# Optimization experiments

Hardware: AMD Instinct MI355X
Metric: run time of the kernel (lower is better)

Reference implementation:

```python
import jax, jax.numpy as jnp
import numpy as np

N_EMBD = 1024
N_HEAD = 16

def _lin_params(key, fan_in, fan_out):
    kw, kb = jax.random.split(key)
    bound = 1.0 / np.sqrt(fan_in)
    W = jax.random.uniform(kw, (fan_in, fan_out), minval=-bound, maxval=bound, dtype=jnp.float32)
    b = jax.random.uniform(kb, (fan_out,), minval=-bound, maxval=bound, dtype=jnp.float32)
    return W, b

def setup_inputs() -> dict:
    key = jax.random.key(0)
    ks = jax.random.split(key, 6)
    x = jax.random.normal(ks[0], (2, 2048, N_EMBD), dtype=jnp.float32)
    W_attn, b_attn = _lin_params(ks[1], N_EMBD, 3 * N_EMBD)
    W_proj, b_proj = _lin_params(ks[2], N_EMBD, N_EMBD)
    W_fc, b_fc = _lin_params(ks[3], N_EMBD, 4 * N_EMBD)
    W_fc2, b_fc2 = _lin_params(ks[4], 4 * N_EMBD, N_EMBD)
    ln1_g = jnp.ones((N_EMBD,), jnp.float32); ln1_b = jnp.zeros((N_EMBD,), jnp.float32)
    ln2_g = jnp.ones((N_EMBD,), jnp.float32); ln2_b = jnp.zeros((N_EMBD,), jnp.float32)
    return {"x": x, "W_attn": W_attn, "b_attn": b_attn, "W_proj": W_proj, "b_proj": b_proj,
            "W_fc": W_fc, "b_fc": b_fc, "W_fc2": W_fc2, "b_fc2": b_fc2,
            "ln1_g": ln1_g, "ln1_b": ln1_b, "ln2_g": ln2_g, "ln2_b": ln2_b}

def _layernorm(x, g, b, eps=1e-5):
    mu = jnp.mean(x, axis=-1, keepdims=True)
    var = jnp.var(x, axis=-1, keepdims=True)
    return (x - mu) * jax.lax.rsqrt(var + eps) * g + b

def _attention(x, W_attn, b_attn, W_proj, b_proj):
    B, T, C = x.shape
    hd = C // N_HEAD
    qkv = x @ W_attn + b_attn                      # [B,T,3C]
    q, k, v = jnp.split(qkv, 3, axis=-1)
    # [B,T,C] -> [B,H,T,hd]
    q = q.reshape(B, T, N_HEAD, hd).transpose(0, 2, 1, 3)
    k = k.reshape(B, T, N_HEAD, hd).transpose(0, 2, 1, 3)
    v = v.reshape(B, T, N_HEAD, hd).transpose(0, 2, 1, 3)
    att = jnp.einsum('bhqd,bhkd->bhqk', q, k) * (1.0 / np.sqrt(hd))
    causal = jnp.tril(jnp.ones((T, T), bool))
    att = jnp.where(causal[None, None], att, -jnp.inf)
    att = jax.nn.softmax(att, axis=-1)
    y = jnp.einsum('bhqk,bhkd->bhqd', att, v)      # [B,H,T,hd]
    y = y.transpose(0, 2, 1, 3).reshape(B, T, C)
    return y @ W_proj + b_proj

def _mlp(x, W_fc, b_fc, W_fc2, b_fc2):
    h = jax.nn.gelu(x @ W_fc + b_fc, approximate=False)
    return h @ W_fc2 + b_fc2

def reference(x, W_attn, b_attn, W_proj, b_proj, W_fc, b_fc, W_fc2, b_fc2,
              ln1_g, ln1_b, ln2_g, ln2_b):
    x = x + _attention(_layernorm(x, ln1_g, ln1_b), W_attn, b_attn, W_proj, b_proj)
    x = x + _mlp(_layernorm(x, ln2_g, ln2_b), W_fc, b_fc, W_fc2, b_fc2)
    return x
```

## Files before the change

kernel.cpp:

```cpp
#include <hip/hip_runtime.h>
#include <cstdint>
#include <cstddef>


typedef unsigned short u16;
typedef short bf16x8 __attribute__((ext_vector_type(8)));
typedef float f32x4 __attribute__((ext_vector_type(4)));

#define C_EMBD 1024
#define T_SEQ  2048
#define N_BATCH 2
#define N_HEADS 16
#define HEAD_D 64
#define M_TOK  4096
#define Q_SCALE 0.18033688011112042f

__device__ __forceinline__ u16 f2b(float f) {
  union { float f; unsigned u; } v; v.f = f;
  unsigned r = (v.u + 0x7fffu + ((v.u >> 16) & 1u)) >> 16;
  return (u16)r;
}
__device__ __forceinline__ float b2f(u16 u) {
  union { unsigned u; float f; } v; v.u = ((unsigned)u) << 16;
  return v.f;
}
__device__ __forceinline__ unsigned pk2(float a, float b) {
  union { float f; unsigned u; } x, y; x.f = a; y.f = b;
  return __builtin_amdgcn_perm(y.u, x.u, 0x07060302u);
}
__device__ __forceinline__ void load_lds16(const void* g, void* l) {
  __builtin_amdgcn_global_load_lds(
      (const __attribute__((address_space(1))) void*)g,
      (__attribute__((address_space(3))) void*)l, 16, 0, 0);
}
__device__ __forceinline__ float gelu_fast(float x) {
  const float p = x * __builtin_fmaf(0.044715f * x, x, 1.0f);
  const float t = __builtin_amdgcn_exp2f(2.3021859215f * p);
  return x * t * __builtin_amdgcn_rcpf(t + 1.0f);
}

__global__ __launch_bounds__(256) void transpose_cast(
    const float* __restrict__ W, u16* __restrict__ Wt, int K, int N) {
  __shared__ float tile[32][33];
  const int n0 = blockIdx.x * 32, k0 = blockIdx.y * 32;
  const int tx = threadIdx.x & 31, ty = threadIdx.x >> 5;
#pragma unroll
  for (int i = 0; i < 32; i += 8)
    tile[ty + i][tx] = W[(size_t)(k0 + ty + i) * N + n0 + tx];
  __syncthreads();
#pragma unroll
  for (int i = 0; i < 32; i += 8)
    Wt[(size_t)(n0 + ty + i) * K + k0 + tx] = f2b(tile[tx][ty + i]);
}

__global__ __launch_bounds__(256) void ln_cast(
    const float* __restrict__ X, const float* __restrict__ g,
    const float* __restrict__ b, u16* __restrict__ Y) {
  const int row = blockIdx.x;
  const int tid = threadIdx.x;
  const float4 v = ((const float4*)(X + (size_t)row * C_EMBD))[tid];
  float s = v.x + v.y + v.z + v.w;
  float ss = v.x * v.x + v.y * v.y + v.z * v.z + v.w * v.w;
#pragma unroll
  for (int off = 32; off > 0; off >>= 1) {
    s += __shfl_down(s, off, 64);
    ss += __shfl_down(ss, off, 64);
  }
  __shared__ float red[8];
  __shared__ float stats[2];
  const int wave = tid >> 6, lane = tid & 63;
  if (lane == 0) { red[wave] = s; red[4 + wave] = ss; }
  __syncthreads();
  if (tid == 0) {
    float S = red[0] + red[1] + red[2] + red[3];
    float SS = red[4] + red[5] + red[6] + red[7];
    float mu = S * (1.0f / C_EMBD);
    float var = SS * (1.0f / C_EMBD) - mu * mu;
    stats[0] = mu;
    stats[1] = rsqrtf(var + 1e-5f);
  }
  __syncthreads();
  const float mu = stats[0], rs = stats[1];
  const float4 gv = ((const float4*)g)[tid];
  const float4 bv = ((const float4*)b)[tid];
  ushort4 o;
  o.x = f2b((v.x - mu) * rs * gv.x + bv.x);
  o.y = f2b((v.y - mu) * rs * gv.y + bv.y);
  o.z = f2b((v.z - mu) * rs * gv.z + bv.z);
  o.w = f2b((v.w - mu) * rs * gv.w + bv.w);
  ((ushort4*)(Y + (size_t)row * C_EMBD))[tid] = o;
}

enum { EPI_BF16 = 0, EPI_GELU_BF16 = 2, EPI_PART = 3, EPI_QKV = 4 };

template <int EPI, int SPLIT>
__global__ __launch_bounds__(256) void gemm_bt(
    const u16* __restrict__ A, const u16* __restrict__ Bt,
    const float* __restrict__ bias,
    void* __restrict__ Cout, void* __restrict__ Cout2, void* __restrict__ Cout3,
    int M, int N, int K) {
  __shared__ u16 As[128 * 64];
  __shared__ u16 Bs[128 * 64];
  const int tid = threadIdx.x;
  const int wave = tid >> 6, lane = tid & 63;
  const int quad = lane >> 4, l16 = lane & 15;
  const int sw = l16 & 7;
  const int m0 = blockIdx.y * 128, n0 = blockIdx.x * 128;
  const int wm = (wave >> 1) * 64, wn = (wave & 1) * 64;

  f32x4 acc[4][4] = {};

  const int kTiles = (K >> 6) / SPLIT;
  const int kt0 = (SPLIT == 2) ? (int)blockIdx.z * kTiles : 0;
  for (int kt = kt0; kt < kt0 + kTiles; ++kt) {
    const int k0 = kt << 6;
#pragma unroll
    for (int i = 0; i < 4; ++i) {
      const int c = tid + i * 256;
      const int row = c >> 3, gc = ((c & 7) ^ (row & 7)) * 8;
      load_lds16(A + (size_t)(m0 + row) * K + k0 + gc, &As[c * 8]);
    }
#pragma unroll
    for (int i = 0; i < 4; ++i) {
      const int c = tid + i * 256;
      const int row = c >> 3, gc = ((c & 7) ^ (row & 7)) * 8;
      load_lds16(Bt + (size_t)(n0 + row) * K + k0 + gc, &Bs[c * 8]);
    }
    __syncthreads();
#pragma unroll
    for (int ks = 0; ks < 2; ++ks) {
      bf16x8 aF[4], bF[4];
#pragma unroll
      for (int t = 0; t < 4; ++t) {
        aF[t] = *(const bf16x8*)
            &As[(wm + t * 16 + l16) * 64 + (((ks * 4 + quad) ^ sw) * 8)];
        bF[t] = *(const bf16x8*)
            &Bs[(wn + t * 16 + l16) * 64 + (((ks * 4 + quad) ^ sw) * 8)];
      }
#pragma unroll
      for (int tm = 0; tm < 4; ++tm)
#pragma unroll
        for (int tn = 0; tn < 4; ++tn)
          acc[tm][tn] = __builtin_amdgcn_mfma_f32_16x16x32_bf16(
              bF[tn], aF[tm], acc[tm][tn], 0, 0, 0);
    }
    __syncthreads();
  }

  float* Pz = (float*)((SPLIT == 2 && blockIdx.z == 1) ? Cout2 : Cout);
#pragma unroll
  for (int tm = 0; tm < 4; ++tm) {
    const int row = m0 + wm + tm * 16 + l16;
#pragma unroll
    for (int tn = 0; tn < 4; ++tn) {
      const int col = n0 + wn + tn * 16 + quad * 4;
      if constexpr (EPI == EPI_PART) {
        *(float4*)&Pz[(size_t)row * N + col] = *(float4*)&acc[tm][tn];
      } else if constexpr (EPI == EPI_QKV) {
        const int bb = row >> 11, t = row & (T_SEQ - 1);
        const float4 bz = *(const float4*)&bias[col];
        float v0 = acc[tm][tn][0] + bz.x, v1 = acc[tm][tn][1] + bz.y;
        float v2 = acc[tm][tn][2] + bz.z, v3 = acc[tm][tn][3] + bz.w;
        const int sec = col >> 10;
        const int h = (col & 1023) >> 6, d4 = col & 63;
        const int bh = bb * N_HEADS + h;
        if (sec == 0) {
          ushort4 o;
          o.x = f2b(v0 * Q_SCALE); o.y = f2b(v1 * Q_SCALE);
          o.z = f2b(v2 * Q_SCALE); o.w = f2b(v3 * Q_SCALE);
          *(ushort4*)&((u16*)Cout)[((size_t)bh * T_SEQ + t) * HEAD_D + d4] = o;
        } else if (sec == 1) {
          ushort4 o;
          o.x = f2b(v0); o.y = f2b(v1); o.z = f2b(v2); o.w = f2b(v3);
          *(ushort4*)&((u16*)Cout2)[((size_t)bh * T_SEQ + t) * HEAD_D + d4] = o;
        } else {
          u16* vp = (u16*)Cout3 + ((size_t)bh * HEAD_D + d4) * T_SEQ + t;
          vp[0] = f2b(v0); vp[T_SEQ] = f2b(v1);
          vp[2 * T_SEQ] = f2b(v2); vp[3 * T_SEQ] = f2b(v3);
        }
      } else {
        const float4 bz = *(const float4*)&bias[col];
        float v0 = acc[tm][tn][0] + bz.x, v1 = acc[tm][tn][1] + bz.y;
        float v2 = acc[tm][tn][2] + bz.z, v3 = acc[tm][tn][3] + bz.w;
        if constexpr (EPI == EPI_GELU_BF16) {
          v0 = gelu_fast(v0); v1 = gelu_fast(v1);
          v2 = gelu_fast(v2); v3 = gelu_fast(v3);
        }
        ushort4 o;
        o.x = f2b(v0); o.y = f2b(v1); o.z = f2b(v2); o.w = f2b(v3);
        *(ushort4*)&((u16*)Cout)[(size_t)row * N + col] = o;
      }
    }
  }
}

__global__ __launch_bounds__(256) void reduce_add(
    const float* __restrict__ P0, const float* __restrict__ P1,
    const float* __restrict__ bias, const float* __restrict__ res,
    float* __restrict__ out) {
  const int idx = blockIdx.x * 256 + threadIdx.x;
  const float4 a = ((const float4*)P0)[idx];
  const float4 b = ((const float4*)P1)[idx];
  const float4 c = ((const float4*)res)[idx];
  const float4 g = ((const float4*)bias)[idx & 255];
  float4 o;
  o.x = a.x + b.x + c.x + g.x;
  o.y = a.y + b.y + c.y + g.y;
  o.z = a.z + b.z + c.z + g.z;
  o.w = a.w + b.w + c.w + g.w;
  ((float4*)out)[idx] = o;
}

__global__ __launch_bounds__(256) void attn_fwd(
    const u16* __restrict__ Q, const u16* __restrict__ Kb,
    const u16* __restrict__ Vt, u16* __restrict__ Y) {
  const int bh = blockIdx.y;
  const int pair = blockIdx.x;
  const int nqt = (int)(T_SEQ / 64);
  const int tid = threadIdx.x;
  const int wave = tid >> 6, lane = tid & 63;
  const int quad = lane >> 4, l16 = lane & 15;
  const int sw = l16 & 7;
  const u16* Qp = Q + (size_t)bh * T_SEQ * HEAD_D;
  const u16* Kp = Kb + (size_t)bh * T_SEQ * HEAD_D;
  const u16* Vp = Vt + (size_t)bh * HEAD_D * T_SEQ;

  __shared__ u16 Ks[2][64 * 64];
  __shared__ u16 Vs[2][64 * 64];
  __shared__ u16 Pl[4][16 * 72];

  const int c1 = tid, c2 = tid + 256;
  const int r1 = c1 >> 3, g1 = ((c1 & 7) ^ (r1 & 7)) * 8;
  const int r2 = c2 >> 3, g2 = ((c2 & 7) ^ (r2 & 7)) * 8;
  const size_t kO1 = (size_t)r1 * HEAD_D + g1, kO2 = (size_t)r2 * HEAD_D + g2;
  const size_t vO1 = (size_t)r1 * T_SEQ + g1, vO2 = (size_t)r2 * T_SEQ + g2;
  u16* const dK1[2] = {&Ks[0][c1 * 8], &Ks[1][c1 * 8]};
  u16* const dK2[2] = {&Ks[0][c2 * 8], &Ks[1][c2 * 8]};
  u16* const dV1[2] = {&Vs[0][c1 * 8], &Vs[1][c1 * 8]};
  u16* const dV2[2] = {&Vs[0][c2 * 8], &Vs[1][c2 * 8]};

  auto stageK = [&](int bb, int k0) {
    const u16* base = Kp + (size_t)k0 * HEAD_D;
    load_lds16(base + kO1, dK1[bb]);
    load_lds16(base + kO2, dK2[bb]);
  };
  auto stageV = [&](int bb, int k0) {
    const u16* base = Vp + k0;
    load_lds16(base + vO1, dV1[bb]);
    load_lds16(base + vO2, dV2[bb]);
  };

  const int b = bh >> 4, h = bh & 15;

#pragma unroll 1
  for (int phase = 0; phase < 2; ++phase) {
    const int qb = phase == 0 ? (nqt - 1 - pair) : pair;
    const int q0 = qb * 64;
    const int qglob = q0 + wave * 16 + l16;

    if (phase == 1) __syncthreads();

    bf16x8 qF[2];
    qF[0] = *(const bf16x8*)&Qp[(size_t)qglob * HEAD_D + quad * 8];
    qF[1] = *(const bf16x8*)&Qp[(size_t)qglob * HEAD_D + 32 + quad * 8];

    f32x4 o[4] = {};
    float mrun = -3e38f, lrun = 0.0f;

    stageK(0, 0);
    stageV(0, 0);

    int buf = 0;
    for (int kb = 0; kb <= qb; ++kb) {
      const int k0 = kb * 64;
      __syncthreads();
      if (kb < qb) {
        stageK(buf ^ 1, k0 + 64);
        stageV(buf ^ 1, k0 + 64);
      }
      f32x4 st[4] = {};
#pragma unroll
      for (int ks = 0; ks < 2; ++ks) {
#pragma unroll
        for (int nt = 0; nt < 4; ++nt) {
          bf16x8 kF = *(const bf16x8*)
              &Ks[buf][(nt * 16 + l16) * 64 + (((ks * 4 + quad) ^ sw) * 8)];
          st[nt] = __builtin_amdgcn_mfma_f32_16x16x32_bf16(kF, qF[ks], st[nt],
                                                           0, 0, 0);
        }
      }
      if (kb == qb) {
#pragma unroll
        for (int nt = 0; nt < 4; ++nt) {
#pragma unroll
          for (int r = 0; r < 4; ++r) {
            const int key = k0 + nt * 16 + quad * 4 + r;
            if (key > qglob) st[nt][r] = -3e38f;
          }
        }
      }
      float m = st[0][0];
#pragma unroll
      for (int nt = 0; nt < 4; ++nt)
#pragma unroll
        for (int r = 0; r < 4; ++r) m = fmaxf(m, st[nt][r]);
      m = fmaxf(m, __shfl_xor(m, 16, 64));
      m = fmaxf(m, __shfl_xor(m, 32, 64));
      const float nm = fmaxf(mrun, m);
      const float alpha = __builtin_amdgcn_exp2f(mrun - nm);
      mrun = nm;
      float sum = 0.0f;
#pragma unroll
      for (int nt = 0; nt < 4; ++nt)
#pragma unroll
        for (int r = 0; r < 4; ++r) {
          const float p = __builtin_amdgcn_exp2f(st[nt][r] - nm);
          st[nt][r] = p;
          sum += p;
        }
      sum += __shfl_xor(sum, 16, 64);
      sum += __shfl_xor(sum, 32, 64);
      lrun = lrun * alpha + sum;
#pragma unroll
      for (int nt = 0; nt < 4; ++nt)
#pragma unroll
        for (int r = 0; r < 4; ++r) o[nt][r] *= alpha;
#pragma unroll
      for (int nt = 0; nt < 4; ++nt) {
        uint2 pk;
        pk.x = pk2(st[nt][0], st[nt][1]);
        pk.y = pk2(st[nt][2], st[nt][3]);
        *(uint2*)&Pl[wave][l16 * 72 + nt * 16 + quad * 4] = pk;
      }
#pragma unroll
      for (int ks = 0; ks < 2; ++ks) {
        bf16x8 aP = *(const bf16x8*)&Pl[wave][l16 * 72 + ks * 32 + quad * 8];
#pragma unroll
        for (int nt = 0; nt < 4; ++nt) {
          bf16x8 vF = *(const bf16x8*)
              &Vs[buf][(nt * 16 + l16) * 64 + (((ks * 4 + quad) ^ sw) * 8)];
          o[nt] =
              __builtin_amdgcn_mfma_f32_16x16x32_bf16(vF, aP, o[nt], 0, 0, 0);
        }
      }
      buf ^= 1;
    }

    const float rl = 1.0f / lrun;
    u16* yp = Y + ((size_t)(b * T_SEQ + qglob)) * C_EMBD + h * HEAD_D;
#pragma unroll
    for (int nt = 0; nt < 4; ++nt) {
      ushort4 ov;
      ov.x = f2b(o[nt][0] * rl); ov.y = f2b(o[nt][1] * rl);
      ov.z = f2b(o[nt][2] * rl); ov.w = f2b(o[nt][3] * rl);
      *(ushort4*)&yp[nt * 16 + quad * 4] = ov;
    }
  }
}

extern "C" void kernel_launch(void* const* d_in, const int* in_sizes, int n_in,
                              void* d_out, int out_size, void* d_ws,
                              size_t ws_size, hipStream_t stream) {
  const float* x      = (const float*)d_in[0];
  const float* W_attn = (const float*)d_in[1];
  const float* b_attn = (const float*)d_in[2];
  const float* W_proj = (const float*)d_in[3];
  const float* b_proj = (const float*)d_in[4];
  const float* W_fc   = (const float*)d_in[5];
  const float* b_fc   = (const float*)d_in[6];
  const float* W_fc2  = (const float*)d_in[7];
  const float* b_fc2  = (const float*)d_in[8];
  const float* ln1_g  = (const float*)d_in[9];
  const float* ln1_b  = (const float*)d_in[10];
  const float* ln2_g  = (const float*)d_in[11];
  const float* ln2_b  = (const float*)d_in[12];

  u16* wqkvT = (u16*)d_ws;
  u16* wprojT = wqkvT + (size_t)3072 * 1024;
  u16* wfcT  = wprojT + (size_t)1024 * 1024;
  u16* wfc2T = wfcT + (size_t)4096 * 1024;
  u16* Abuf  = wfc2T + (size_t)1024 * 4096;
  float* x1  = (float*)(Abuf + (size_t)M_TOK * C_EMBD);
  u16* hbuf  = (u16*)(x1 + (size_t)M_TOK * C_EMBD);
  float* projP = (float*)hbuf;
  u16* Qb    = hbuf + (size_t)M_TOK * 4096;
  u16* Kbuf  = Qb + (size_t)32 * T_SEQ * HEAD_D;
  u16* Vtb   = Kbuf + (size_t)32 * T_SEQ * HEAD_D;
  float* fc2P1 = (float*)Qb;

  const dim3 blk(256);

  transpose_cast<<<dim3(3072 / 32, 1024 / 32), blk, 0, stream>>>(W_attn, wqkvT, 1024, 3072);
  transpose_cast<<<dim3(1024 / 32, 1024 / 32), blk, 0, stream>>>(W_proj, wprojT, 1024, 1024);
  transpose_cast<<<dim3(4096 / 32, 1024 / 32), blk, 0, stream>>>(W_fc, wfcT, 1024, 4096);
  transpose_cast<<<dim3(1024 / 32, 4096 / 32), blk, 0, stream>>>(W_fc2, wfc2T, 4096, 1024);

  ln_cast<<<M_TOK, blk, 0, stream>>>(x, ln1_g, ln1_b, Abuf);

  gemm_bt<EPI_QKV, 1><<<dim3(3072 / 128, M_TOK / 128), blk, 0, stream>>>(
      Abuf, wqkvT, b_attn, Qb, Kbuf, Vtb, M_TOK, 3072, 1024);

  attn_fwd<<<dim3(T_SEQ / 128, 32), blk, 0, stream>>>(Qb, Kbuf, Vtb, Abuf);

  gemm_bt<EPI_PART, 2><<<dim3(1024 / 128, M_TOK / 128, 2), blk, 0, stream>>>(
      Abuf, wprojT, nullptr, projP, projP + (size_t)M_TOK * C_EMBD, nullptr,
      M_TOK, 1024, 1024);
  reduce_add<<<M_TOK * C_EMBD / 1024, blk, 0, stream>>>(
      projP, projP + (size_t)M_TOK * C_EMBD, b_proj, x, x1);

  ln_cast<<<M_TOK, blk, 0, stream>>>(x1, ln2_g, ln2_b, Abuf);

  gemm_bt<EPI_GELU_BF16, 1><<<dim3(4096 / 128, M_TOK / 128), blk, 0, stream>>>(
      Abuf, wfcT, b_fc, hbuf, nullptr, nullptr, M_TOK, 4096, 1024);

  gemm_bt<EPI_PART, 2><<<dim3(1024 / 128, M_TOK / 128, 2), blk, 0, stream>>>(
      hbuf, wfc2T, nullptr, d_out, fc2P1, nullptr, M_TOK, 1024, 4096);
  reduce_add<<<M_TOK * C_EMBD / 1024, blk, 0, stream>>>(
      (const float*)d_out, fc2P1, b_fc2, x1, (float*)d_out);
}
```

Measured before the change: 362.2 us.

## Fuse split-K reduce with LayerNorm and group GEMM tiles along M

```diff
diff --git a/kernel.cpp b/kernel.cpp
--- a/kernel.cpp
+++ b/kernel.cpp
@@ -91,6 +91,56 @@
   ((ushort4*)(Y + (size_t)row * C_EMBD))[tid] = o;
 }
 
+__global__ __launch_bounds__(256) void ln_reduce_cast(
+    const float* __restrict__ P0, const float* __restrict__ P1,
+    const float* __restrict__ bias, const float* __restrict__ res,
+    const float* __restrict__ g, const float* __restrict__ b,
+    float* __restrict__ X1, u16* __restrict__ Y) {
+  const int row = blockIdx.x;
+  const int tid = threadIdx.x;
+  const size_t base = (size_t)row * C_EMBD;
+  const float4 p0 = ((const float4*)(P0 + base))[tid];
+  const float4 p1 = ((const float4*)(P1 + base))[tid];
+  const float4 rr = ((const float4*)(res + base))[tid];
+  const float4 bb = ((const float4*)bias)[tid];
+  float4 v;
+  v.x = p0.x + p1.x + rr.x + bb.x;
+  v.y = p0.y + p1.y + rr.y + bb.y;
+  v.z = p0.z + p1.z + rr.z + bb.z;
+  v.w = p0.w + p1.w + rr.w + bb.w;
+  ((float4*)(X1 + base))[tid] = v;
+  float s = v.x + v.y + v.z + v.w;
+  float ss = v.x * v.x + v.y * v.y + v.z * v.z + v.w * v.w;
+#pragma unroll
+  for (int off = 32; off > 0; off >>= 1) {
+    s += __shfl_down(s, off, 64);
+    ss += __shfl_down(ss, off, 64);
+  }
+  __shared__ float red[8];
+  __shared__ float stats[2];
+  const int wave = tid >> 6, lane = tid & 63;
+  if (lane == 0) { red[wave] = s; red[4 + wave] = ss; }
+  __syncthreads();
+  if (tid == 0) {
+    float S = red[0] + red[1] + red[2] + red[3];
+    float SS = red[4] + red[5] + red[6] + red[7];
+    float mu = S * (1.0f / C_EMBD);
+    float var = SS * (1.0f / C_EMBD) - mu * mu;
+    stats[0] = mu;
+    stats[1] = rsqrtf(var + 1e-5f);
+  }
+  __syncthreads();
+  const float mu = stats[0], rs = stats[1];
+  const float4 gv = ((const float4*)g)[tid];
+  const float4 bv = ((const float4*)b)[tid];
+  ushort4 o;
+  o.x = f2b((v.x - mu) * rs * gv.x + bv.x);
+  o.y = f2b((v.y - mu) * rs * gv.y + bv.y);
+  o.z = f2b((v.z - mu) * rs * gv.z + bv.z);
+  o.w = f2b((v.w - mu) * rs * gv.w + bv.w);
+  ((ushort4*)(Y + base))[tid] = o;
+}
+
 enum { EPI_BF16 = 0, EPI_GELU_BF16 = 2, EPI_PART = 3, EPI_QKV = 4 };
 
 template <int EPI, int SPLIT>
@@ -105,7 +155,14 @@
   const int wave = tid >> 6, lane = tid & 63;
   const int quad = lane >> 4, l16 = lane & 15;
   const int sw = l16 & 7;
-  const int m0 = blockIdx.y * 128, n0 = blockIdx.x * 128;
+
+  const int nBx = (int)gridDim.x;
+  const int id = (int)blockIdx.y * nBx + (int)blockIdx.x;
+  const int span = 8 * nBx;
+  const int gid = id / span, rem = id % span;
+  const int mt = gid * 8 + (rem & 7), nt_ = rem >> 3;
+  const int m0 = mt * 128, n0 = nt_ * 128;
+
   const int wm = (wave >> 1) * 64, wn = (wave & 1) * 64;
 
   f32x4 acc[4][4] = {};
@@ -405,10 +462,9 @@
   gemm_bt<EPI_PART, 2><<<dim3(1024 / 128, M_TOK / 128, 2), blk, 0, stream>>>(
       Abuf, wprojT, nullptr, projP, projP + (size_t)M_TOK * C_EMBD, nullptr,
       M_TOK, 1024, 1024);
-  reduce_add<<<M_TOK * C_EMBD / 1024, blk, 0, stream>>>(
-      projP, projP + (size_t)M_TOK * C_EMBD, b_proj, x, x1);
-
-  ln_cast<<<M_TOK, blk, 0, stream>>>(x1, ln2_g, ln2_b, Abuf);
+  ln_reduce_cast<<<M_TOK, blk, 0, stream>>>(
+      projP, projP + (size_t)M_TOK * C_EMBD, b_proj, x, ln2_g, ln2_b,
+      x1, Abuf);
 
   gemm_bt<EPI_GELU_BF16, 1><<<dim3(4096 / 128, M_TOK / 128), blk, 0, stream>>>(
       Abuf, wfcT, b_fc, hbuf, nullptr, nullptr, M_TOK, 4096, 1024);
```

Result: faster. 353.8 us (-2.3%).
